# Optimization experiments

Hardware: AMD Instinct MI355X
Metric: run time of the kernel (lower is better)

## Reference

```python
import jax, jax.numpy as jnp
import numpy as np

N, V, E_PER = 8, 4608, 73728          # batch, nodes per graph, edges per graph
D_IN, C, NCLS = 1, 512, 3             # node feat dim, embed dim, classes
E = N * E_PER
LN_EPS = 1e-5


def setup_inputs() -> dict:
    key = jax.random.key(0)
    ks = jax.random.split(key, 12)
    x = jax.random.normal(ks[0], (N, 1, V, D_IN), jnp.float32)
    edge_index = jax.random.randint(ks[1], (2, E), 0, V, dtype=jnp.int32)
    edge_weight = jax.random.uniform(ks[2], (E,), jnp.float32)
    # GCNConv params: layer0 maps D_IN->C, layers 1..2 map C->C (weight [in,out], bias [out])
    w0 = jax.random.normal(ks[3], (D_IN, C), jnp.float32) * 0.02
    b0 = jnp.zeros((C,), jnp.float32)
    w1 = jax.random.normal(ks[4], (C, C), jnp.float32) * 0.02
    b1 = jnp.zeros((C,), jnp.float32)
    w2 = jax.random.normal(ks[5], (C, C), jnp.float32) * 0.02
    b2 = jnp.zeros((C,), jnp.float32)
    ln_g = jnp.ones((C,), jnp.float32)
    ln_b = jnp.zeros((C,), jnp.float32)
    head_w = jax.random.normal(ks[6], (C, NCLS), jnp.float32) * 2e-5
    head_b = jnp.log(jnp.full((NCLS,), 1.0 / NCLS, jnp.float32))
    return {"x": x, "edge_weight": edge_weight, "w0": w0, "b0": b0,
            "w1": w1, "b1": b1, "w2": w2, "b2": b2,
            "ln_g": ln_g, "ln_b": ln_b, "head_w": head_w, "head_b": head_b,
            "edge_index": edge_index}


def layer_norm(h, g, b):
    mu = h.mean(-1, keepdims=True)
    var = ((h - mu) ** 2).mean(-1, keepdims=True)
    return (h - mu) * jax.lax.rsqrt(var + LN_EPS) * g + b


def reference(x, edge_weight, w0, b0, w1, b1, w2, b2, ln_g, ln_b, head_w, head_b, edge_index):
    n, t, v, d = x.shape
    nv = n * v
    h = x.reshape(nv, d)
    # batch-offset local edge indices (edges are contiguous per graph)
    offs = jnp.repeat(jnp.arange(n, dtype=edge_index.dtype) * v, edge_index.shape[1] // n)
    src = edge_index[0] + offs
    tgt = edge_index[1] + offs
    # GCN norm with self-loops (fill weight 1.0), symmetric deg^-1/2 normalization
    loop = jnp.arange(nv, dtype=src.dtype)
    src_f = jnp.concatenate([src, loop])
    tgt_f = jnp.concatenate([tgt, loop])
    ew_f = jnp.concatenate([edge_weight, jnp.ones((nv,), edge_weight.dtype)])
    deg = jax.ops.segment_sum(ew_f, tgt_f, num_segments=nv)
    deg_safe = jnp.where(deg > 0, deg, 1.0)
    dinv = jnp.where(deg > 0, jax.lax.rsqrt(deg_safe), 0.0)
    norm = dinv[src_f] * ew_f * dinv[tgt_f]
    for w, bb in ((w0, b0), (w1, b1), (w2, b2)):
        hw = h @ w                                   # [NV, C]
        msg = norm[:, None] * hw[src_f]              # gather + scale  [E+NV, C]
        h = jax.ops.segment_sum(msg, tgt_f, num_segments=nv) + bb
        h = jax.nn.relu(h)
        h = layer_norm(h, ln_g, ln_b)
        # dropout is identity in eval mode
    pooled = h.reshape(n, v, -1).max(axis=1)         # global_max_pool (contiguous batch)
    pooled = layer_norm(pooled, ln_g, ln_b)
    return pooled @ head_w + head_b                  # [N, NCLS]
```

## Files before the change

kernel.cpp:

```cpp
#include <hip/hip_runtime.h>
#include <hip/hip_bf16.h>
#include <stdint.h>

#define N_GRAPH 8
#define V_NODES 4608
#define E_PER   73728
#define NV      (N_GRAPH * V_NODES)
#define E_TOT   (N_GRAPH * E_PER)
#define C       512
#define NCLS    3
#define LN_EPS  1e-5f
#define POOL_CHUNKS 36
#define SCAN_BLOCKS 144
#define SUBB    32
#define EPSB    (E_PER / SUBB)

typedef __attribute__((ext_vector_type(8))) short short8;
typedef __attribute__((ext_vector_type(4))) float floatx4;
typedef __attribute__((address_space(1))) void v_g;
typedef __attribute__((address_space(3))) void v_l;


__device__ inline float waveReduceSum(float v) {
#pragma unroll
    for (int o = 32; o > 0; o >>= 1) v += __shfl_down(v, o, 64);
    return v;
}

__device__ inline float waveAllSum(float v) {
#pragma unroll
    for (int o = 32; o > 0; o >>= 1) v += __shfl_xor(v, o, 64);
    return v;
}

__device__ inline float blockSum512(float v, volatile float* sred) {
    float s = waveReduceSum(v);
    if ((threadIdx.x & 63) == 0) sred[threadIdx.x >> 6] = s;
    __syncthreads();
    float t = 0.f;
#pragma unroll
    for (int i = 0; i < 8; i++) t += sred[i];
    __syncthreads();
    return t;
}

__device__ inline unsigned short f2bf(float f) {
    uint32_t u = __float_as_uint(f);
    u += 0x7fffu + ((u >> 16) & 1u);
    return (unsigned short)(u >> 16);
}
__device__ inline float bf2f(unsigned short b) {
    return __uint_as_float(((uint32_t)b) << 16);
}


__launch_bounds__(256)
__global__ void k_hist(const int* __restrict__ ei, const float* __restrict__ ew,
                       int* __restrict__ hist_c, float* __restrict__ hist_d) {
    __shared__ int   lcnt[V_NODES];
    __shared__ float ldeg[V_NODES];
    const int g = blockIdx.x >> 5, j = blockIdx.x & 31;
    const int tid = threadIdx.x;
    for (int i = tid; i < V_NODES; i += 256) { lcnt[i] = 0; ldeg[i] = 0.f; }
    __syncthreads();
    const int ebase = g * E_PER + j * EPSB;
    const int*   tgt = ei + E_TOT + ebase;
    const float* w   = ew + ebase;
    for (int i = tid; i < EPSB; i += 256) {
        int t = tgt[i];
        atomicAdd(&lcnt[t], 1);
        atomicAdd(&ldeg[t], w[i]);
    }
    __syncthreads();
    const size_t hb = ((size_t)g * SUBB + j) * V_NODES;
    for (int i = tid; i < V_NODES; i += 256) {
        hist_c[hb + i] = lcnt[i];
        hist_d[hb + i] = ldeg[i];
    }
}

__global__ void k_reduce(int* __restrict__ hist_c, const float* __restrict__ hist_d,
                         int* __restrict__ counts, float* __restrict__ dinv) {
    const int node = blockIdx.x * 256 + threadIdx.x;
    if (node >= NV) return;
    const int g = node / V_NODES, t = node - g * V_NODES;
    const size_t base = (size_t)g * SUBB * V_NODES + t;
    int c = 0;
    float d = 1.0f;
#pragma unroll 8
    for (int j = 0; j < SUBB; j++) {
        const size_t idx = base + (size_t)j * V_NODES;
        int cc = hist_c[idx];
        hist_c[idx] = c;
        c += cc;
        d += hist_d[idx];
    }
    counts[node] = c;
    dinv[node] = rsqrtf(d);
}


__global__ void k_scan1(const int* __restrict__ counts, int* __restrict__ row_ptr,
                        int* __restrict__ bsum) {
    __shared__ int sh[256];
    const int b = blockIdx.x, tid = threadIdx.x;
    const int idx = b * 256 + tid;
    int v = counts[idx];
    sh[tid] = v;
    __syncthreads();
#pragma unroll
    for (int off = 1; off < 256; off <<= 1) {
        int t = (tid >= off) ? sh[tid - off] : 0;
        __syncthreads();
        sh[tid] += t;
        __syncthreads();
    }
    row_ptr[idx] = sh[tid] - v;
    if (tid == 255) bsum[b] = sh[255];
}

__global__ void k_scan2(int* __restrict__ bsum) {
    __shared__ int sh[256];
    const int tid = threadIdx.x;
    int v = (tid < SCAN_BLOCKS) ? bsum[tid] : 0;
    sh[tid] = v;
    __syncthreads();
#pragma unroll
    for (int off = 1; off < 256; off <<= 1) {
        int t = (tid >= off) ? sh[tid - off] : 0;
        __syncthreads();
        sh[tid] += t;
        __syncthreads();
    }
    if (tid < SCAN_BLOCKS) bsum[tid] = sh[tid] - v;
}

__global__ void k_scan3(int* __restrict__ row_ptr, const int* __restrict__ bsum) {
    const int b = blockIdx.x, tid = threadIdx.x;
    const int idx = b * 256 + tid;
    row_ptr[idx] += bsum[b];
    if (idx == 0) row_ptr[NV] = E_TOT;
}

__launch_bounds__(256)
__global__ void k_fill2(const int* __restrict__ ei, const float* __restrict__ ew,
                        const float* __restrict__ dinv, const int* __restrict__ row_ptr,
                        const int* __restrict__ hist_c,
                        int* __restrict__ col_idx, float* __restrict__ val) {
    __shared__ int cur[V_NODES];
    const int g = blockIdx.x >> 5, j = blockIdx.x & 31;
    const int tid = threadIdx.x;
    const int gV = g * V_NODES;
    const size_t hb = ((size_t)g * SUBB + j) * V_NODES;
    for (int i = tid; i < V_NODES; i += 256)
        cur[i] = row_ptr[gV + i] + hist_c[hb + i];
    __syncthreads();
    const int ebase = g * E_PER + j * EPSB;
    const int*   src = ei + ebase;
    const int*   tgt = ei + E_TOT + ebase;
    const float* w   = ew + ebase;
    for (int i = tid; i < EPSB; i += 256) {
        int t = tgt[i];
        int s = src[i] + gV;
        int pos = atomicAdd(&cur[t], 1);
        col_idx[pos] = s;
        val[pos] = dinv[s] * w[i] * dinv[gV + t];
    }
}


__global__ void k_wt(const float* __restrict__ w1, const float* __restrict__ w2,
                     unsigned short* __restrict__ wt1, unsigned short* __restrict__ wt2) {
    int idx = blockIdx.x * 256 + threadIdx.x;
    int which = idx >> 18;
    int rem = idx & 0x3ffff;
    int n = rem >> 9, k = rem & 511;
    const float* W = which ? w2 : w1;
    unsigned short* WT = which ? wt2 : wt1;
    WT[n * C + k] = f2bf(W[k * C + n]);
}


__global__ void k_agg0_scalar(const float* __restrict__ x, const int* __restrict__ row_ptr,
                              const int* __restrict__ col_idx, const float* __restrict__ val,
                              const float* __restrict__ dinv, float* __restrict__ s0) {
    int t = blockIdx.x * 256 + threadIdx.x;
    if (t >= NV) return;
    float dt = dinv[t];
    float acc = dt * dt * x[t];
    int e1 = row_ptr[t + 1];
    for (int e = row_ptr[t]; e < e1; e++)
        acc += val[e] * x[col_idx[e]];
    s0[t] = acc;
}

__launch_bounds__(128)
__global__ void k_l0post(const float* __restrict__ s0, const float* __restrict__ w0,
                         const float* __restrict__ b0, const float* __restrict__ ln_g,
                         const float* __restrict__ ln_b, unsigned short* __restrict__ out) {
    const int t = blockIdx.x;
    const int tid = threadIdx.x;
    const int c4 = tid << 2;
    float s = s0[t];
    float4 w = *reinterpret_cast<const float4*>(&w0[c4]);
    float4 bb = *reinterpret_cast<const float4*>(&b0[c4]);
    float vx = fmaxf(s * w.x + bb.x, 0.f);
    float vy = fmaxf(s * w.y + bb.y, 0.f);
    float vz = fmaxf(s * w.z + bb.z, 0.f);
    float vw = fmaxf(s * w.w + bb.w, 0.f);
    __shared__ float redA[2], redB[2];
    float wsum = waveReduceSum(vx + vy + vz + vw);
    if ((tid & 63) == 0) redA[tid >> 6] = wsum;
    __syncthreads();
    float mu = (redA[0] + redA[1]) * (1.0f / C);
    float dx = vx - mu, dy = vy - mu, dz = vz - mu, dw = vw - mu;
    float wsq = waveReduceSum(dx * dx + dy * dy + dz * dz + dw * dw);
    if ((tid & 63) == 0) redB[tid >> 6] = wsq;
    __syncthreads();
    float rstd = rsqrtf((redB[0] + redB[1]) * (1.0f / C) + LN_EPS);
    float4 g = *reinterpret_cast<const float4*>(&ln_g[c4]);
    float4 b = *reinterpret_cast<const float4*>(&ln_b[c4]);
    ushort4 o = { f2bf(dx * rstd * g.x + b.x), f2bf(dy * rstd * g.y + b.y),
                  f2bf(dz * rstd * g.z + b.z), f2bf(dw * rstd * g.w + b.w) };
    reinterpret_cast<ushort4*>(out)[(size_t)t * 128 + tid] = o;
}


__launch_bounds__(256)
__global__ void k_gemm_mfma(const unsigned short* __restrict__ A,
                            const unsigned short* __restrict__ WT,
                            unsigned short* __restrict__ Bout) {
    __shared__ short8 lA[512];
    __shared__ short8 lB[512];
    const int tid = threadIdx.x;
    const int lane = tid & 63;
    const int wave = tid >> 6;
    const int wr = wave >> 1, wc = wave & 1;
    const int l15 = lane & 15, kg = lane >> 4;
    const int m0 = blockIdx.x * 128;
    const int n0 = blockIdx.y * 128;

    floatx4 acc[4][4] = {};

    const int s0i = tid, s1i = 256 + tid;
    const int kgs0 = s0i >> 7, idx0 = s0i & 127;
    const int kgs1 = s1i >> 7, idx1 = s1i & 127;
    const unsigned short* gA0 = A + (size_t)(m0 + idx0) * C + kgs0 * 8;
    const unsigned short* gA1 = A + (size_t)(m0 + idx1) * C + kgs1 * 8;
    const unsigned short* gB0 = WT + (size_t)(n0 + idx0) * C + kgs0 * 8;
    const unsigned short* gB1 = WT + (size_t)(n0 + idx1) * C + kgs1 * 8;

    for (int k0 = 0; k0 < C; k0 += 32) {
        __builtin_amdgcn_global_load_lds((v_g*)(gA0 + k0), (v_l*)&lA[s0i], 16, 0, 0);
        __builtin_amdgcn_global_load_lds((v_g*)(gA1 + k0), (v_l*)&lA[s1i], 16, 0, 0);
        __builtin_amdgcn_global_load_lds((v_g*)(gB0 + k0), (v_l*)&lB[s0i], 16, 0, 0);
        __builtin_amdgcn_global_load_lds((v_g*)(gB1 + k0), (v_l*)&lB[s1i], 16, 0, 0);
        asm volatile("s_waitcnt vmcnt(0)" ::: "memory");
        __syncthreads();

        short8 af[4], bf[4];
#pragma unroll
        for (int mi = 0; mi < 4; mi++)
            af[mi] = lA[kg * 128 + wr * 64 + mi * 16 + l15];
#pragma unroll
        for (int ni = 0; ni < 4; ni++)
            bf[ni] = lB[kg * 128 + wc * 64 + ni * 16 + l15];
#pragma unroll
        for (int mi = 0; mi < 4; mi++)
#pragma unroll
            for (int ni = 0; ni < 4; ni++)
                acc[mi][ni] = __builtin_amdgcn_mfma_f32_16x16x32_bf16(
                    af[mi], bf[ni], acc[mi][ni], 0, 0, 0);
        __syncthreads();
    }

#pragma unroll
    for (int mi = 0; mi < 4; mi++) {
#pragma unroll
        for (int ni = 0; ni < 4; ni++) {
            int n = n0 + wc * 64 + ni * 16 + l15;
#pragma unroll
            for (int r = 0; r < 4; r++) {
                int m = m0 + wr * 64 + mi * 16 + kg * 4 + r;
                Bout[(size_t)m * C + n] = f2bf(acc[mi][ni][r]);
            }
        }
    }
}


__launch_bounds__(256)
__global__ void k_agg(const unsigned short* __restrict__ hw, const int* __restrict__ row_ptr,
                      const int* __restrict__ col_idx, const float* __restrict__ val,
                      const float* __restrict__ dinv, const float* __restrict__ bias,
                      const float* __restrict__ ln_g, const float* __restrict__ ln_b,
                      unsigned short* __restrict__ out) {
    const int b = blockIdx.x;
    const int wv = threadIdx.x >> 6;
    const int lane = threadIdx.x & 63;
    const int t = (b & 7) * V_NODES + ((b >> 3) << 2) + wv;
    const int e0 = row_ptr[t], e1 = row_ptr[t + 1];
    const short8* hw8 = reinterpret_cast<const short8*>(hw);

    const float dt = dinv[t];
    const float selfw = dt * dt;
    short8 hs = hw8[(size_t)t * 64 + lane];
    float a[8];
#pragma unroll
    for (int i = 0; i < 8; i++) a[i] = selfw * bf2f((unsigned short)hs[i]);

    int e = e0;
    for (; e + 4 <= e1; e += 4) {
        int i0 = col_idx[e], i1 = col_idx[e + 1], i2 = col_idx[e + 2], i3 = col_idx[e + 3];
        float w0 = val[e], w1 = val[e + 1], w2 = val[e + 2], w3 = val[e + 3];
        short8 h0 = hw8[(size_t)i0 * 64 + lane];
        short8 h1 = hw8[(size_t)i1 * 64 + lane];
        short8 h2 = hw8[(size_t)i2 * 64 + lane];
        short8 h3 = hw8[(size_t)i3 * 64 + lane];
#pragma unroll
        for (int i = 0; i < 8; i++) a[i] += w0 * bf2f((unsigned short)h0[i]);
#pragma unroll
        for (int i = 0; i < 8; i++) a[i] += w1 * bf2f((unsigned short)h1[i]);
#pragma unroll
        for (int i = 0; i < 8; i++) a[i] += w2 * bf2f((unsigned short)h2[i]);
#pragma unroll
        for (int i = 0; i < 8; i++) a[i] += w3 * bf2f((unsigned short)h3[i]);
    }
    for (; e < e1; e++) {
        int is = col_idx[e];
        float w = val[e];
        short8 hv = hw8[(size_t)is * 64 + lane];
#pragma unroll
        for (int i = 0; i < 8; i++) a[i] += w * bf2f((unsigned short)hv[i]);
    }

    const int c8 = lane << 3;
    float4 bb0 = *reinterpret_cast<const float4*>(&bias[c8]);
    float4 bb1 = *reinterpret_cast<const float4*>(&bias[c8 + 4]);
    a[0] = fmaxf(a[0] + bb0.x, 0.f); a[1] = fmaxf(a[1] + bb0.y, 0.f);
    a[2] = fmaxf(a[2] + bb0.z, 0.f); a[3] = fmaxf(a[3] + bb0.w, 0.f);
    a[4] = fmaxf(a[4] + bb1.x, 0.f); a[5] = fmaxf(a[5] + bb1.y, 0.f);
    a[6] = fmaxf(a[6] + bb1.z, 0.f); a[7] = fmaxf(a[7] + bb1.w, 0.f);

    float s = a[0] + a[1] + a[2] + a[3] + a[4] + a[5] + a[6] + a[7];
    float mu = waveAllSum(s) * (1.0f / C);
    float sq = 0.f;
#pragma unroll
    for (int i = 0; i < 8; i++) { float d = a[i] - mu; sq += d * d; }
    float rstd = rsqrtf(waveAllSum(sq) * (1.0f / C) + LN_EPS);

    float4 g0 = *reinterpret_cast<const float4*>(&ln_g[c8]);
    float4 g1 = *reinterpret_cast<const float4*>(&ln_g[c8 + 4]);
    float4 z0 = *reinterpret_cast<const float4*>(&ln_b[c8]);
    float4 z1 = *reinterpret_cast<const float4*>(&ln_b[c8 + 4]);
    short8 o;
    o[0] = (short)f2bf((a[0] - mu) * rstd * g0.x + z0.x);
    o[1] = (short)f2bf((a[1] - mu) * rstd * g0.y + z0.y);
    o[2] = (short)f2bf((a[2] - mu) * rstd * g0.z + z0.z);
    o[3] = (short)f2bf((a[3] - mu) * rstd * g0.w + z0.w);
    o[4] = (short)f2bf((a[4] - mu) * rstd * g1.x + z1.x);
    o[5] = (short)f2bf((a[5] - mu) * rstd * g1.y + z1.y);
    o[6] = (short)f2bf((a[6] - mu) * rstd * g1.z + z1.z);
    o[7] = (short)f2bf((a[7] - mu) * rstd * g1.w + z1.w);
    reinterpret_cast<short8*>(out)[(size_t)t * 64 + lane] = o;
}


__global__ void k_pool1(const unsigned short* __restrict__ h, float* __restrict__ pmax) {
    int g = blockIdx.x, chunk = blockIdx.y;
    int c = threadIdx.x;
    int r0 = g * V_NODES + chunk * 128;
    float m = -1e30f;
#pragma unroll 4
    for (int r = 0; r < 128; r++)
        m = fmaxf(m, bf2f(h[(size_t)(r0 + r) * C + c]));
    pmax[((size_t)g * POOL_CHUNKS + chunk) * C + c] = m;
}

__global__ void k_pool2_head(const float* __restrict__ pmax, const float* __restrict__ ln_g,
                             const float* __restrict__ ln_b, const float* __restrict__ hw,
                             const float* __restrict__ hb, float* __restrict__ out) {
    __shared__ float sred[8];
    int g = blockIdx.x;
    int c = threadIdx.x;
    float m = -1e30f;
#pragma unroll
    for (int j = 0; j < POOL_CHUNKS; j++)
        m = fmaxf(m, pmax[((size_t)g * POOL_CHUNKS + j) * C + c]);
    float total = blockSum512(m, sred);
    float mu = total * (1.0f / C);
    float d = m - mu;
    float var = blockSum512(d * d, sred) * (1.0f / C);
    float rstd = rsqrtf(var + LN_EPS);
    float p = d * rstd * ln_g[c] + ln_b[c];
    float r0 = blockSum512(p * hw[c * NCLS + 0], sred);
    float r1 = blockSum512(p * hw[c * NCLS + 1], sred);
    float r2 = blockSum512(p * hw[c * NCLS + 2], sred);
    if (threadIdx.x == 0) {
        out[g * NCLS + 0] = r0 + hb[0];
        out[g * NCLS + 1] = r1 + hb[1];
        out[g * NCLS + 2] = r2 + hb[2];
    }
}


extern "C" void kernel_launch(void* const* d_in, const int* in_sizes, int n_in,
                              void* d_out, int out_size, void* d_ws, size_t ws_size,
                              hipStream_t stream) {
    const float* x      = (const float*)d_in[0];
    const float* ew     = (const float*)d_in[1];
    const float* w0     = (const float*)d_in[2];
    const float* b0     = (const float*)d_in[3];
    const float* w1     = (const float*)d_in[4];
    const float* b1     = (const float*)d_in[5];
    const float* w2     = (const float*)d_in[6];
    const float* b2     = (const float*)d_in[7];
    const float* ln_g   = (const float*)d_in[8];
    const float* ln_b   = (const float*)d_in[9];
    const float* head_w = (const float*)d_in[10];
    const float* head_b = (const float*)d_in[11];
    const int*   ei     = (const int*)d_in[12];
    float* out = (float*)d_out;

    char* p = (char*)d_ws;
    auto alloc = [&](size_t bytes) { void* r = p; p += (bytes + 255) & ~255ull; return r; };
    unsigned short* bufA = (unsigned short*)alloc((size_t)NV * C * 2);
    unsigned short* bufB = (unsigned short*)alloc((size_t)NV * C * 2);
    unsigned short* wt1  = (unsigned short*)alloc((size_t)C * C * 2);
    unsigned short* wt2  = (unsigned short*)alloc((size_t)C * C * 2);
    float* s0      = (float*)alloc((size_t)NV * 4);
    float* dinv    = (float*)alloc((size_t)NV * 4);
    int*   counts  = (int*)alloc((size_t)NV * 4);
    int*   row_ptr = (int*)alloc((size_t)(NV + 1) * 4);
    int*   bsum    = (int*)alloc((size_t)SCAN_BLOCKS * 4);
    int*   hist_c  = (int*)alloc((size_t)N_GRAPH * SUBB * V_NODES * 4);
    float* hist_d  = (float*)alloc((size_t)N_GRAPH * SUBB * V_NODES * 4);
    int*   col_idx = (int*)alloc((size_t)E_TOT * 4);
    float* val     = (float*)alloc((size_t)E_TOT * 4);
    float* pmax    = (float*)alloc((size_t)N_GRAPH * POOL_CHUNKS * C * 4);

    k_hist<<<N_GRAPH * SUBB, 256, 0, stream>>>(ei, ew, hist_c, hist_d);
    k_reduce<<<SCAN_BLOCKS, 256, 0, stream>>>(hist_c, hist_d, counts, dinv);
    k_scan1<<<SCAN_BLOCKS, 256, 0, stream>>>(counts, row_ptr, bsum);
    k_scan2<<<1, 256, 0, stream>>>(bsum);
    k_scan3<<<SCAN_BLOCKS, 256, 0, stream>>>(row_ptr, bsum);
    k_fill2<<<N_GRAPH * SUBB, 256, 0, stream>>>(ei, ew, dinv, row_ptr, hist_c, col_idx, val);
    k_wt<<<(2 * C * C) / 256, 256, 0, stream>>>(w1, w2, wt1, wt2);

    k_agg0_scalar<<<NV / 256, 256, 0, stream>>>(x, row_ptr, col_idx, val, dinv, s0);
    k_l0post<<<NV, 128, 0, stream>>>(s0, w0, b0, ln_g, ln_b, bufA);

    k_gemm_mfma<<<dim3(NV / 128, C / 128), 256, 0, stream>>>(bufA, wt1, bufB);
    k_agg<<<NV / 4, 256, 0, stream>>>(bufB, row_ptr, col_idx, val, dinv, b1, ln_g, ln_b, bufA);

    k_gemm_mfma<<<dim3(NV / 128, C / 128), 256, 0, stream>>>(bufA, wt2, bufB);
    k_agg<<<NV / 4, 256, 0, stream>>>(bufB, row_ptr, col_idx, val, dinv, b2, ln_g, ln_b, bufA);

    k_pool1<<<dim3(N_GRAPH, POOL_CHUNKS), C, 0, stream>>>(bufA, pmax);
    k_pool2_head<<<N_GRAPH, C, 0, stream>>>(pmax, ln_g, ln_b, head_w, head_b, out);
}
```

Baseline: 375.7 us.

## Store GEMM output in FP8 to halve gather traffic in aggregation

The GEMM epilogue now packs its results into FP8 (e4m3) bytes instead of bf16, and the aggregation kernel gathers 8-byte FP8 rows per lane and unpacks them with the hardware conversion builtins. This halves the bytes moved by the dominant random neighbour gathers and the GEMM stores. In exchange it adds quantisation error, which LayerNorm may partly absorb but could break tolerance. The pool kernel is also rewritten with vectorised short8 reads per wave and more partial maxima.

```diff
diff --git a/kernel.cpp b/kernel.cpp
--- a/kernel.cpp
+++ b/kernel.cpp
@@ -11,12 +11,14 @@
 #define NCLS    3
 #define LN_EPS  1e-5f
 #define POOL_CHUNKS 36
+#define POOL_PARTS  144
 #define SCAN_BLOCKS 144
 #define SUBB    32
 #define EPSB    (E_PER / SUBB)
 
 typedef __attribute__((ext_vector_type(8))) short short8;
 typedef __attribute__((ext_vector_type(4))) float floatx4;
+typedef __attribute__((ext_vector_type(2))) float float2v;
 typedef __attribute__((address_space(1))) void v_g;
 typedef __attribute__((address_space(3))) void v_l;
 
@@ -52,6 +54,58 @@
 __device__ inline float bf2f(unsigned short b) {
     return __uint_as_float(((uint32_t)b) << 16);
 }
+
+
+#if __has_builtin(__builtin_amdgcn_cvt_pk_fp8_f32)
+__device__ inline uint32_t pk_fp8(float a, float b) {
+    return (uint32_t)__builtin_amdgcn_cvt_pk_fp8_f32(a, b, 0, false);
+}
+#else
+__device__ inline uint32_t fp8_enc1(float f) {
+    float a = fminf(fmaxf(f, -448.f), 448.f);
+    uint32_t u = __float_as_uint(a);
+    uint32_t s = (u >> 24) & 0x80;
+    int e = (int)((u >> 23) & 0xff) - 127;
+    uint32_t m = u & 0x7fffff;
+    if (a == 0.f || e < -9) return s;
+    if (e < -6) {
+        int sh = -6 - e;
+        uint32_t full = 0x800000u | m;
+        uint32_t q = full >> (20 + sh);
+        uint32_t rem = full & ((1u << (20 + sh)) - 1);
+        uint32_t half = 1u << (19 + sh);
+        q += (rem > half || (rem == half && (q & 1)));
+        return s | q;
+    }
+    uint32_t q = m >> 20;
+    uint32_t rem = m & 0xfffff;
+    q += (rem > 0x80000 || (rem == 0x80000 && (q & 1)));
+    uint32_t v = ((uint32_t)(e + 7) << 3) + q;
+    if (v > 0x7e) v = 0x7e;
+    return s | v;
+}
+__device__ inline uint32_t pk_fp8(float a, float b) {
+    return fp8_enc1(a) | (fp8_enc1(b) << 8);
+}
+#endif
+
+#if __has_builtin(__builtin_amdgcn_cvt_pk_f32_fp8)
+__device__ inline float2v up_fp8_lo(uint32_t w) { return __builtin_amdgcn_cvt_pk_f32_fp8((int)w, false); }
+__device__ inline float2v up_fp8_hi(uint32_t w) { return __builtin_amdgcn_cvt_pk_f32_fp8((int)w, true); }
+#else
+__device__ inline float fp8_dec1(uint32_t b) {
+    uint32_t s = (b >> 7) & 1u, e = (b >> 3) & 0xfu, m = b & 7u;
+    float mag = e ? ldexpf(1.0f + (float)m * 0.125f, (int)e - 7)
+                  : (float)m * 0.001953125f;
+    return s ? -mag : mag;
+}
+__device__ inline float2v up_fp8_lo(uint32_t w) {
+    float2v r; r.x = fp8_dec1(w & 0xff); r.y = fp8_dec1((w >> 8) & 0xff); return r;
+}
+__device__ inline float2v up_fp8_hi(uint32_t w) {
+    float2v r; r.x = fp8_dec1((w >> 16) & 0xff); r.y = fp8_dec1(w >> 24); return r;
+}
+#endif
 
 
 __launch_bounds__(256)
@@ -229,7 +283,7 @@
 __launch_bounds__(256)
 __global__ void k_gemm_mfma(const unsigned short* __restrict__ A,
                             const unsigned short* __restrict__ WT,
-                            unsigned short* __restrict__ Bout) {
+                            uint8_t* __restrict__ Bout) {
     __shared__ short8 lA[512];
     __shared__ short8 lB[512];
     const int tid = threadIdx.x;
@@ -279,18 +333,21 @@
 #pragma unroll
         for (int ni = 0; ni < 4; ni++) {
             int n = n0 + wc * 64 + ni * 16 + l15;
-#pragma unroll
-            for (int r = 0; r < 4; r++) {
-                int m = m0 + wr * 64 + mi * 16 + kg * 4 + r;
-                Bout[(size_t)m * C + n] = f2bf(acc[mi][ni][r]);
-            }
+            floatx4 v = acc[mi][ni];
+            uint32_t p01 = pk_fp8(v[0], v[1]);
+            uint32_t p23 = pk_fp8(v[2], v[3]);
+            uint8_t* rp = Bout + (size_t)(m0 + wr * 64 + mi * 16 + kg * 4) * C + n;
+            rp[0]     = (uint8_t)p01;
+            rp[C]     = (uint8_t)(p01 >> 8);
+            rp[2 * C] = (uint8_t)p23;
+            rp[3 * C] = (uint8_t)(p23 >> 8);
         }
     }
 }
 
 
 __launch_bounds__(256)
-__global__ void k_agg(const unsigned short* __restrict__ hw, const int* __restrict__ row_ptr,
+__global__ void k_agg(const uint8_t* __restrict__ hw, const int* __restrict__ row_ptr,
                       const int* __restrict__ col_idx, const float* __restrict__ val,
                       const float* __restrict__ dinv, const float* __restrict__ bias,
                       const float* __restrict__ ln_g, const float* __restrict__ ln_b,
@@ -300,39 +357,45 @@
     const int lane = threadIdx.x & 63;
     const int t = (b & 7) * V_NODES + ((b >> 3) << 2) + wv;
     const int e0 = row_ptr[t], e1 = row_ptr[t + 1];
-    const short8* hw8 = reinterpret_cast<const short8*>(hw);
+    const uint2* hw8 = reinterpret_cast<const uint2*>(hw);
 
     const float dt = dinv[t];
     const float selfw = dt * dt;
-    short8 hs = hw8[(size_t)t * 64 + lane];
     float a[8];
-#pragma unroll
-    for (int i = 0; i < 8; i++) a[i] = selfw * bf2f((unsigned short)hs[i]);
+    {
+        uint2 hv = hw8[(size_t)t * 64 + lane];
+        float2v f01 = up_fp8_lo(hv.x), f23 = up_fp8_hi(hv.x);
+        float2v f45 = up_fp8_lo(hv.y), f67 = up_fp8_hi(hv.y);
+        a[0] = selfw * f01.x; a[1] = selfw * f01.y;
+        a[2] = selfw * f23.x; a[3] = selfw * f23.y;
+        a[4] = selfw * f45.x; a[5] = selfw * f45.y;
+        a[6] = selfw * f67.x; a[7] = selfw * f67.y;
+    }
 
     int e = e0;
     for (; e + 4 <= e1; e += 4) {
         int i0 = col_idx[e], i1 = col_idx[e + 1], i2 = col_idx[e + 2], i3 = col_idx[e + 3];
         float w0 = val[e], w1 = val[e + 1], w2 = val[e + 2], w3 = val[e + 3];
-        short8 h0 = hw8[(size_t)i0 * 64 + lane];
-        short8 h1 = hw8[(size_t)i1 * 64 + lane];
-        short8 h2 = hw8[(size_t)i2 * 64 + lane];
-        short8 h3 = hw8[(size_t)i3 * 64 + lane];
-#pragma unroll
-        for (int i = 0; i < 8; i++) a[i] += w0 * bf2f((unsigned short)h0[i]);
-#pragma unroll
-        for (int i = 0; i < 8; i++) a[i] += w1 * bf2f((unsigned short)h1[i]);
-#pragma unroll
-        for (int i = 0; i < 8; i++) a[i] += w2 * bf2f((unsigned short)h2[i]);
-#pragma unroll
-        for (int i = 0; i < 8; i++) a[i] += w3 * bf2f((unsigned short)h3[i]);
+        uint2 h0 = hw8[(size_t)i0 * 64 + lane];
+        uint2 h1 = hw8[(size_t)i1 * 64 + lane];
+        uint2 h2 = hw8[(size_t)i2 * 64 + lane];
+        uint2 h3 = hw8[(size_t)i3 * 64 + lane];
+#define ACC8(hv, w) { \
+        float2v q01 = up_fp8_lo(hv.x), q23 = up_fp8_hi(hv.x); \
+        float2v q45 = up_fp8_lo(hv.y), q67 = up_fp8_hi(hv.y); \
+        a[0] += (w) * q01.x; a[1] += (w) * q01.y; \
+        a[2] += (w) * q23.x; a[3] += (w) * q23.y; \
+        a[4] += (w) * q45.x; a[5] += (w) * q45.y; \
+        a[6] += (w) * q67.x; a[7] += (w) * q67.y; }
+        ACC8(h0, w0) ACC8(h1, w1) ACC8(h2, w2) ACC8(h3, w3)
     }
     for (; e < e1; e++) {
         int is = col_idx[e];
         float w = val[e];
-        short8 hv = hw8[(size_t)is * 64 + lane];
-#pragma unroll
-        for (int i = 0; i < 8; i++) a[i] += w * bf2f((unsigned short)hv[i]);
-    }
+        uint2 hv = hw8[(size_t)is * 64 + lane];
+        ACC8(hv, w)
+    }
+#undef ACC8
 
     const int c8 = lane << 3;
     float4 bb0 = *reinterpret_cast<const float4*>(&bias[c8]);
@@ -366,15 +429,25 @@
 }
 
 
+__launch_bounds__(256)
 __global__ void k_pool1(const unsigned short* __restrict__ h, float* __restrict__ pmax) {
-    int g = blockIdx.x, chunk = blockIdx.y;
-    int c = threadIdx.x;
-    int r0 = g * V_NODES + chunk * 128;
-    float m = -1e30f;
-#pragma unroll 4
-    for (int r = 0; r < 128; r++)
-        m = fmaxf(m, bf2f(h[(size_t)(r0 + r) * C + c]));
-    pmax[((size_t)g * POOL_CHUNKS + chunk) * C + c] = m;
+    const int g = blockIdx.x, chunk = blockIdx.y;
+    const int wv = threadIdx.x >> 6, lane = threadIdx.x & 63;
+    const short8* h8 = reinterpret_cast<const short8*>(h);
+    const size_t r0 = (size_t)g * V_NODES + chunk * 128 + wv * 32;
+    float m[8];
+#pragma unroll
+    for (int i = 0; i < 8; i++) m[i] = -1e30f;
+    for (int r = 0; r < 32; r++) {
+        short8 v = h8[(r0 + r) * 64 + lane];
+#pragma unroll
+        for (int i = 0; i < 8; i++) m[i] = fmaxf(m[i], bf2f((unsigned short)v[i]));
+    }
+    float* dst = pmax + ((size_t)(g * POOL_PARTS + chunk * 4 + wv)) * C + (lane << 3);
+    float4 o0 = { m[0], m[1], m[2], m[3] };
+    float4 o1 = { m[4], m[5], m[6], m[7] };
+    *reinterpret_cast<float4*>(dst) = o0;
+    *reinterpret_cast<float4*>(dst + 4) = o1;
 }
 
 __global__ void k_pool2_head(const float* __restrict__ pmax, const float* __restrict__ ln_g,
@@ -384,9 +457,8 @@
     int g = blockIdx.x;
     int c = threadIdx.x;
     float m = -1e30f;
-#pragma unroll
-    for (int j = 0; j < POOL_CHUNKS; j++)
-        m = fmaxf(m, pmax[((size_t)g * POOL_CHUNKS + j) * C + c]);
+    for (int j = 0; j < POOL_PARTS; j++)
+        m = fmaxf(m, pmax[((size_t)g * POOL_PARTS + j) * C + c]);
     float total = blockSum512(m, sred);
     float mu = total * (1.0f / C);
     float d = m - mu;
@@ -425,7 +497,7 @@
     char* p = (char*)d_ws;
     auto alloc = [&](size_t bytes) { void* r = p; p += (bytes + 255) & ~255ull; return r; };
     unsigned short* bufA = (unsigned short*)alloc((size_t)NV * C * 2);
-    unsigned short* bufB = (unsigned short*)alloc((size_t)NV * C * 2);
+    uint8_t*        bufF = (uint8_t*)alloc((size_t)NV * C);
     unsigned short* wt1  = (unsigned short*)alloc((size_t)C * C * 2);
     unsigned short* wt2  = (unsigned short*)alloc((size_t)C * C * 2);
     float* s0      = (float*)alloc((size_t)NV * 4);
@@ -437,7 +509,7 @@
     float* hist_d  = (float*)alloc((size_t)N_GRAPH * SUBB * V_NODES * 4);
     int*   col_idx = (int*)alloc((size_t)E_TOT * 4);
     float* val     = (float*)alloc((size_t)E_TOT * 4);
-    float* pmax    = (float*)alloc((size_t)N_GRAPH * POOL_CHUNKS * C * 4);
+    float* pmax    = (float*)alloc((size_t)N_GRAPH * POOL_PARTS * C * 4);
 
     k_hist<<<N_GRAPH * SUBB, 256, 0, stream>>>(ei, ew, hist_c, hist_d);
     k_reduce<<<SCAN_BLOCKS, 256, 0, stream>>>(hist_c, hist_d, counts, dinv);
@@ -450,12 +522,12 @@
     k_agg0_scalar<<<NV / 256, 256, 0, stream>>>(x, row_ptr, col_idx, val, dinv, s0);
     k_l0post<<<NV, 128, 0, stream>>>(s0, w0, b0, ln_g, ln_b, bufA);
 
-    k_gemm_mfma<<<dim3(NV / 128, C / 128), 256, 0, stream>>>(bufA, wt1, bufB);
-    k_agg<<<NV / 4, 256, 0, stream>>>(bufB, row_ptr, col_idx, val, dinv, b1, ln_g, ln_b, bufA);
-
-    k_gemm_mfma<<<dim3(NV / 128, C / 128), 256, 0, stream>>>(bufA, wt2, bufB);
-    k_agg<<<NV / 4, 256, 0, stream>>>(bufB, row_ptr, col_idx, val, dinv, b2, ln_g, ln_b, bufA);
-
-    k_pool1<<<dim3(N_GRAPH, POOL_CHUNKS), C, 0, stream>>>(bufA, pmax);
+    k_gemm_mfma<<<dim3(NV / 128, C / 128), 256, 0, stream>>>(bufA, wt1, bufF);
+    k_agg<<<NV / 4, 256, 0, stream>>>(bufF, row_ptr, col_idx, val, dinv, b1, ln_g, ln_b, bufA);
+
+    k_gemm_mfma<<<dim3(NV / 128, C / 128), 256, 0, stream>>>(bufA, wt2, bufF);
+    k_agg<<<NV / 4, 256, 0, stream>>>(bufF, row_ptr, col_idx, val, dinv, b2, ln_g, ln_b, bufA);
+
+    k_pool1<<<dim3(N_GRAPH, POOL_CHUNKS), 256, 0, stream>>>(bufA, pmax);
     k_pool2_head<<<N_GRAPH, C, 0, stream>>>(pmax, ln_g, ln_b, head_w, head_b, out);
 }
```

Result: no change. 369.4 us (-1.7%).
